# Kernel tuning notes

Measured on AMD Instinct MI355X. Metric: run time of the kernel, lower is better.

The kernel has to match this reference:

```python
import jax, jax.numpy as jnp
import numpy as np
import math

D_MODEL = 1024
D_STATE = 64
DT_MIN = 0.001
DT_MAX = 0.1
BATCH = 4
SEQLEN = 4096


def make_hippo_matrix(N):
    P = np.sqrt(1 + 2 * np.arange(N))
    A = P[:, np.newaxis] * P[np.newaxis, :]
    A = np.tril(A) - np.diag(np.arange(N))
    return jnp.asarray(-A, dtype=jnp.float32)


def setup_inputs() -> dict:
    key = jax.random.key(0)
    k_u, k_B, k_C, k_D, k_dt = jax.random.split(key, 5)
    u = jax.random.normal(k_u, (BATCH, SEQLEN, D_MODEL), dtype=jnp.float32)
    A = make_hippo_matrix(D_STATE)  # (N, N) HiPPO-LegS buffer
    B = jax.random.normal(k_B, (D_STATE, 1), dtype=jnp.float32)
    C = jax.random.normal(k_C, (1, D_STATE), dtype=jnp.float32)
    D = jax.random.normal(k_D, (1,), dtype=jnp.float32)
    log_dt = (jax.random.uniform(k_dt, (1,), dtype=jnp.float32)
              * (math.log(DT_MAX) - math.log(DT_MIN)) + math.log(DT_MIN))
    return {"u": u, "A": A, "B": B, "C": C, "D": D, "log_dt": log_dt}


def _forward(u, A, B, C, D, log_dt):
    n = A.shape[0]
    dt = jnp.exp(log_dt)[0]
    A_bar = jax.scipy.linalg.expm(dt * A)                     # (N, N)
    B_bar = jnp.linalg.solve(A, (A_bar - jnp.eye(n, dtype=A.dtype)) @ B)  # (N, 1)
    bvec = B_bar[:, 0]          # (N,)
    cvec = C[0]                 # (N,)
    d_scalar = D[0]
    # Faithful to source: only channel 0 of u drives the SSM.
    u0 = u[:, :, 0]             # (Bn, L)

    def step(x, u_t):
        # x: (Bn, N), u_t: (Bn,)
        x = x @ A_bar.T + u_t[:, None] * bvec
        y = x @ cvec + d_scalar * u_t   # (Bn,)
        return x, y

    x0 = jnp.zeros((u.shape[0], n), dtype=u.dtype)
    _, ys = jax.lax.scan(step, x0, jnp.swapaxes(u0, 0, 1))   # (L, Bn)
    # Scalar output broadcast across all H channels (matches torch expand)
    y = jnp.broadcast_to(jnp.swapaxes(ys, 0, 1)[:, :, None], u.shape)
    return y


def reference(u, A, B, C, D, log_dt):
    return _forward(u, A, B, C, D, log_dt)
```

## Files before the change

### kernel.cpp

```cpp
#include <hip/hip_runtime.h>


#define NT 256
#define MP 68
#define MB (64 * MP)

typedef __attribute__((ext_vector_type(8))) short v8s;
typedef __attribute__((ext_vector_type(4))) float v4f;

__device__ __forceinline__ unsigned short bf16r(float x) {
  union { float f; unsigned u; } v; v.f = x;
  unsigned r = v.u + 0x7fffu + ((v.u >> 16) & 1u);
  return (unsigned short)(r >> 16);
}
__device__ __forceinline__ float bf2f(unsigned short h) {
  union { unsigned u; float f; } v; v.u = ((unsigned)h) << 16;
  return v.f;
}
__device__ __forceinline__ void cvt4(const float4 f, ushort4* H, ushort4* L) {
  unsigned short h;
  h = bf16r(f.x); H->x = h; L->x = bf16r(f.x - bf2f(h));
  h = bf16r(f.y); H->y = h; L->y = bf16r(f.y - bf2f(h));
  h = bf16r(f.z); H->z = h; L->z = bf16r(f.z - bf2f(h));
  h = bf16r(f.w); H->w = h; L->w = bf16r(f.w - bf2f(h));
}

__device__ void mm(const float* Ag, const float* Bs, int bT,
                   float* Cd, int cpitch, float* Cd2,
                   int nrt, int nct, int rowbase, int colbase,
                   unsigned short* FRAG) {
  const int t = threadIdx.x;
  __syncthreads();
  for (int s0 = 0; s0 < 512; s0 += 256) {
    const int s = s0 + t;
    const int l = s & 63, Tq = s >> 6;
    const int mrow = (Tq >> 1) * 16 + (l & 15);
    const int kk = (Tq & 1) * 32 + (l >> 4) * 8;
    const float* ap = Ag + mrow * MP + kk;
    const float4 f0 = *(const float4*)ap;
    const float4 f1 = *(const float4*)(ap + 4);
    ushort4 H0, L0, H1, L1;
    cvt4(f0, &H0, &L0); cvt4(f1, &H1, &L1);
    *(ushort4*)(FRAG + s * 8)            = H0;
    *(ushort4*)(FRAG + s * 8 + 4)        = H1;
    *(ushort4*)(FRAG + 4096 + s * 8)     = L0;
    *(ushort4*)(FRAG + 4096 + s * 8 + 4) = L1;
    float4 g0, g1;
    if (bT) {
      const float* bp = Bs + mrow * MP + kk;
      g0 = *(const float4*)bp;
      g1 = *(const float4*)(bp + 4);
    } else {
      g0.x = Bs[(kk + 0) * MP + mrow]; g0.y = Bs[(kk + 1) * MP + mrow];
      g0.z = Bs[(kk + 2) * MP + mrow]; g0.w = Bs[(kk + 3) * MP + mrow];
      g1.x = Bs[(kk + 4) * MP + mrow]; g1.y = Bs[(kk + 5) * MP + mrow];
      g1.z = Bs[(kk + 6) * MP + mrow]; g1.w = Bs[(kk + 7) * MP + mrow];
    }
    cvt4(g0, &H0, &L0); cvt4(g1, &H1, &L1);
    *(ushort4*)(FRAG + 8192 + s * 8)      = H0;
    *(ushort4*)(FRAG + 8192 + s * 8 + 4)  = H1;
    *(ushort4*)(FRAG + 12288 + s * 8)     = L0;
    *(ushort4*)(FRAG + 12288 + s * 8 + 4) = L1;
  }
  __syncthreads();
  {
    const int w = t >> 6, l = t & 63;
    if (w < nrt) {
      const v8s Ah0 = *(const v8s*)(FRAG + ((w * 2 + 0) * 64 + l) * 8);
      const v8s Ah1 = *(const v8s*)(FRAG + ((w * 2 + 1) * 64 + l) * 8);
      const v8s Al0 = *(const v8s*)(FRAG + 4096 + ((w * 2 + 0) * 64 + l) * 8);
      const v8s Al1 = *(const v8s*)(FRAG + 4096 + ((w * 2 + 1) * 64 + l) * 8);
      for (int Cc = 0; Cc < nct; ++Cc) {
        const v8s Bh0 = *(const v8s*)(FRAG + 8192 + ((Cc * 2 + 0) * 64 + l) * 8);
        const v8s Bh1 = *(const v8s*)(FRAG + 8192 + ((Cc * 2 + 1) * 64 + l) * 8);
        const v8s Bl0 = *(const v8s*)(FRAG + 12288 + ((Cc * 2 + 0) * 64 + l) * 8);
        const v8s Bl1 = *(const v8s*)(FRAG + 12288 + ((Cc * 2 + 1) * 64 + l) * 8);
        const v4f z = {0.f, 0.f, 0.f, 0.f};
        v4f a0 = __builtin_amdgcn_mfma_f32_16x16x32_bf16(Ah0, Bh0, z, 0, 0, 0);
        a0 = __builtin_amdgcn_mfma_f32_16x16x32_bf16(Ah1, Bh1, a0, 0, 0, 0);
        v4f a1 = __builtin_amdgcn_mfma_f32_16x16x32_bf16(Ah0, Bl0, z, 0, 0, 0);
        a1 = __builtin_amdgcn_mfma_f32_16x16x32_bf16(Ah1, Bl1, a1, 0, 0, 0);
        v4f a2 = __builtin_amdgcn_mfma_f32_16x16x32_bf16(Al0, Bh0, z, 0, 0, 0);
        a2 = __builtin_amdgcn_mfma_f32_16x16x32_bf16(Al1, Bh1, a2, 0, 0, 0);
        const int col = colbase + Cc * 16 + (l & 15);
        const int r0 = rowbase + w * 16 + (l >> 4) * 4;
        const float o0 = a0[0] + a1[0] + a2[0];
        const float o1 = a0[1] + a1[1] + a2[1];
        const float o2 = a0[2] + a1[2] + a2[2];
        const float o3 = a0[3] + a1[3] + a2[3];
        Cd[(r0 + 0) * cpitch + col] = o0;
        Cd[(r0 + 1) * cpitch + col] = o1;
        Cd[(r0 + 2) * cpitch + col] = o2;
        Cd[(r0 + 3) * cpitch + col] = o3;
        if (Cd2) {
          Cd2[(r0 + 0) * MP + col] = o0;
          Cd2[(r0 + 1) * MP + col] = o1;
          Cd2[(r0 + 2) * MP + col] = o2;
          Cd2[(r0 + 3) * MP + col] = o3;
        }
      }
    }
  }
  __syncthreads();
}

__device__ __forceinline__ void mv64row(const float* M, const float* vin,
                                        float* vout, float* out2, int half) {
  const int t = threadIdx.x;
  __syncthreads();
  const int w = t >> 6, l = t & 63;
  const int row = w * 16 + (l >> 2), q = l & 3;
  const float* mp = M + row * MP + q * 16;
  const float* vp = vin + q * 16;
  float p = 0.f;
#pragma unroll
  for (int j = 0; j < 16; j += 4) {
    const float4 m = *(const float4*)(mp + j);
    p = fmaf(m.x, vp[j + 0], p);
    p = fmaf(m.y, vp[j + 1], p);
    p = fmaf(m.z, vp[j + 2], p);
    p = fmaf(m.w, vp[j + 3], p);
  }
  p += __shfl_xor(p, 1);
  p += __shfl_xor(p, 2);
  if (q == 0) {
    float s = half ? 0.5f * (p + vin[row]) : p;
    vout[row] = s;
    if (out2) out2[row] = s;
  }
  __syncthreads();
}

__device__ __forceinline__ void mv64colT(const float* M, const float* vin,
                                         float* vout, float* out2) {
  const int t = threadIdx.x;
  __syncthreads();
  const int w = t >> 6, l = t & 63;
  const int col = w * 16 + (l >> 2), q = l & 3;
  float p = 0.f;
#pragma unroll
  for (int j = 0; j < 16; ++j)
    p = fmaf(M[(q * 16 + j) * MP + col], vin[q * 16 + j], p);
  p += __shfl_xor(p, 1);
  p += __shfl_xor(p, 2);
  if (q == 0) {
    vout[col] = p;
    if (out2) out2[col] = p;
  }
  __syncthreads();
}

__device__ void buildG(float* dst, const float* X, const float* X2, const float* X3,
                       float c0, float c1, float c2, float c3, const float* addsrc) {
  const int t = threadIdx.x;
  __syncthreads();
  const int r = t >> 2, cb = (t & 3) * 16;
#pragma unroll
  for (int j = 0; j < 16; j += 4) {
    const int c = cb + j;
    const int e = r * MP + c;
    const float4 x1 = *(const float4*)(X + e);
    const float4 x2 = *(const float4*)(X2 + e);
    const float4 x3 = *(const float4*)(X3 + e);
    float4 v;
    v.x = fmaf(c1, x1.x, fmaf(c2, x2.x, c3 * x3.x));
    v.y = fmaf(c1, x1.y, fmaf(c2, x2.y, c3 * x3.y));
    v.z = fmaf(c1, x1.z, fmaf(c2, x2.z, c3 * x3.z));
    v.w = fmaf(c1, x1.w, fmaf(c2, x2.w, c3 * x3.w));
    if (r == c + 0) v.x += c0;
    if (r == c + 1) v.y += c0;
    if (r == c + 2) v.z += c0;
    if (r == c + 3) v.w += c0;
    if (addsrc) {
      const float4 a = *(const float4*)(addsrc + e);
      v.x += a.x; v.y += a.y; v.z += a.z; v.w += a.w;
    }
    *(float4*)(dst + e) = v;
  }
  __syncthreads();
}

__global__ __launch_bounds__(NT) void s4_setup(const float* __restrict__ u,
    const float* __restrict__ A, const float* __restrict__ Bv,
    const float* __restrict__ Cv, const float* __restrict__ logdt,
    float* __restrict__ ws) {
  if (blockIdx.x > 0) {
    const int idx = (blockIdx.x - 1) * NT + threadIdx.x;
    ws[4096 + idx] = u[(size_t)idx * 1024];
    return;
  }
  __shared__ __align__(16) float S0[MB];
  __shared__ __align__(16) unsigned short FRAG[16384];
  __shared__ float vB[64], v1[64], v2[64], v3[64], va[64], vb[64], vg[64];
  __shared__ int s_s;
  float* vscr = (float*)FRAG;

  const int t = threadIdx.x;
  float* kbuf = ws;
  float* gX   = ws + 20480;
  float* gX2  = ws + 24832;
  float* gX3  = ws + 29184;
  float* gU0  = ws + 33536;
  float* gU1  = ws + 37888;
  float* gBRT = ws + 42240;
  float* gCQT = ws + 46592;
  const float dt = expf(logdt[0]);

  const float invf[17] = {1.f, 1.f, 1.f / 2.f, 1.f / 6.f, 1.f / 24.f, 1.f / 120.f,
                          1.f / 720.f, 1.f / 5040.f, 1.f / 40320.f, 1.f / 362880.f,
                          1.f / 3628800.f, 1.f / 39916800.f, 1.f / 479001600.f,
                          1.f / 6.2270208e9f, 1.f / 8.71782912e10f,
                          1.f / 1.307674368e12f, 1.f / 2.0922789888e13f};

  {
    const int j = t & 63, w = t >> 6;
    float p = 0.f;
#pragma unroll
    for (int ii = 0; ii < 16; ++ii) p += fabsf(A[(w * 16 + ii) * 64 + j]);
    vscr[t] = p;
    __syncthreads();
    if (t < 64) {
      float cs = vscr[t] + vscr[64 + t] + vscr[128 + t] + vscr[192 + t];
      cs *= dt;
#pragma unroll
      for (int off = 32; off > 0; off >>= 1) cs = fmaxf(cs, __shfl_xor(cs, off));
      if (t == 0) {
        int s = 0;
        while (cs > 2.0f && s < 30) { cs *= 0.5f; ++s; }
        s_s = s;
      }
    }
    __syncthreads();
  }
  const int sq = s_s;
  const float scl = ldexpf(dt, -sq);

  {
    const int r = t >> 2, cb = (t & 3) * 16;
#pragma unroll
    for (int j = 0; j < 16; j += 4) {
      const float4 a4 = *(const float4*)(A + r * 64 + cb + j);
      float4 x;
      x.x = a4.x * scl; x.y = a4.y * scl; x.z = a4.z * scl; x.w = a4.w * scl;
      *(float4*)(S0 + r * MP + cb + j) = x;
      *(float4*)(gX + r * MP + cb + j) = x;
    }
    if (t < 64) vB[t] = Bv[t];
    __syncthreads();
  }

  mm(S0, S0, 0, S0, MP, gX2, 4, 4, 0, 0, FRAG);
  mm(gX, S0, 0, gX3, MP, nullptr, 4, 4, 0, 0, FRAG);
  mm(S0, S0, 0, S0, MP, nullptr, 4, 4, 0, 0, FRAG);

  mv64row(gX,  vB, v1, nullptr, 0);
  mv64row(gX2, vB, v2, nullptr, 0);
  mv64row(gX3, vB, v3, nullptr, 0);
  if (t < 64)
    va[t] = invf[13] * vB[t] + invf[14] * v1[t] + invf[15] * v2[t] + invf[16] * v3[t];
  __syncthreads();
  mv64row(S0, va, vb, nullptr, 0);
  if (t < 64)
    va[t] = invf[9] * vB[t] + invf[10] * v1[t] + invf[11] * v2[t] + invf[12] * v3[t] + vb[t];
  __syncthreads();
  mv64row(S0, va, vb, nullptr, 0);
  if (t < 64)
    va[t] = invf[5] * vB[t] + invf[6] * v1[t] + invf[7] * v2[t] + invf[8] * v3[t] + vb[t];
  __syncthreads();
  mv64row(S0, va, vb, nullptr, 0);
  if (t < 64)
    vg[t] = invf[1] * vB[t] + invf[2] * v1[t] + invf[3] * v2[t] + invf[4] * v3[t] + vb[t];
  __syncthreads();

  buildG(gU0, gX, gX2, gX3, invf[12], invf[13], invf[14], invf[15], nullptr);
  mm(gU0, S0, 0, gU1, MP, nullptr, 4, 4, 0, 0, FRAG);
  buildG(gU1, gX, gX2, gX3, invf[8], invf[9], invf[10], invf[11], gU1);
  mm(gU1, S0, 0, gU0, MP, nullptr, 4, 4, 0, 0, FRAG);
  buildG(gU0, gX, gX2, gX3, invf[4], invf[5], invf[6], invf[7], gU0);
  mm(gU0, S0, 0, S0, MP, nullptr, 4, 4, 0, 0, FRAG);
  buildG(S0, gX, gX2, gX3, invf[0], invf[1], invf[2], invf[3], S0);

  float* vcur = vg;
  float* vnxt = va;
  for (int it = 0; it < sq; ++it) {
    mv64row(S0, vcur, vnxt, nullptr, 1);
    { float* tmp = vcur; vcur = vnxt; vnxt = tmp; }
    mm(S0, S0, 0, S0, MP, nullptr, 4, 4, 0, 0, FRAG);
  }

  if (t < 64) {
    const float bb = dt * vcur[t];
    v1[t] = bb;
    gBRT[t] = bb;
  }
  __syncthreads();
  {
    float* vc = v1; float* vn = v2;
    for (int r = 1; r < 16; ++r) {
      mv64row(S0, vc, vn, gBRT + r * MP, 0);
      float* tmp = vc; vc = vn; vn = tmp;
    }
  }

  mm(S0, S0, 0, S0, MP, nullptr, 4, 4, 0, 0, FRAG);
  mm(S0, S0, 0, S0, MP, nullptr, 4, 4, 0, 0, FRAG);
  mm(S0, S0, 0, S0, MP, nullptr, 4, 4, 0, 0, FRAG);
  mm(S0, S0, 0, S0, MP, nullptr, 4, 4, 0, 0, FRAG);
  mm(gBRT, S0, 1, gBRT, MP, nullptr, 1, 4, 16, 0, FRAG);
  mm(S0, S0, 0, S0, MP, nullptr, 4, 4, 0, 0, FRAG);
  mm(gBRT, S0, 1, gBRT, MP, nullptr, 2, 4, 32, 0, FRAG);
  mm(S0, S0, 0, S0, MP, nullptr, 4, 4, 0, 0, FRAG);

  if (t < 64) {
    const float cc = Cv[t];
    v1[t] = cc;
    gCQT[t] = cc;
  }
  __syncthreads();
  {
    float* vc = v1; float* vn = v2;
    for (int qx = 1; qx < 16; ++qx) {
      mv64colT(S0, vc, vn, gCQT + qx * MP);
      float* tmp = vc; vc = vn; vn = tmp;
    }
  }

  mm(S0, S0, 0, S0, MP, nullptr, 4, 4, 0, 0, FRAG);
  mm(S0, S0, 0, S0, MP, nullptr, 4, 4, 0, 0, FRAG);
  mm(S0, S0, 0, S0, MP, nullptr, 4, 4, 0, 0, FRAG);
  mm(S0, S0, 0, S0, MP, nullptr, 4, 4, 0, 0, FRAG);
  mm(gCQT, S0, 0, gCQT, MP, nullptr, 1, 4, 16, 0, FRAG);
  mm(S0, S0, 0, S0, MP, nullptr, 4, 4, 0, 0, FRAG);
  mm(gCQT, S0, 0, gCQT, MP, nullptr, 2, 4, 32, 0, FRAG);

  mm(gCQT, gBRT, 1, kbuf, 64, nullptr, 4, 4, 0, 0, FRAG);
}

__global__ __launch_bounds__(256) void s4_out(const float* __restrict__ ws,
                                              const float* __restrict__ Dp,
                                              float* __restrict__ out) {
  const int bid = blockIdx.x;
  const int b = bid >> 10;
  const int t0 = (bid & 1023) << 2;
  const float* kb = ws;
  const float* ub = ws + 4096 + (b << 12);
  const int tid = threadIdx.x;

  float a0 = 0.f, a1 = 0.f, a2 = 0.f, a3 = 0.f;
  for (int s0 = tid << 2; s0 <= t0; s0 += 1024) {
    const float4 uv = *(const float4*)(ub + s0);
    const int b0 = t0 - s0;
    const float4 k0 = *(const float4*)(kb + b0);
    float4 k1 = make_float4(0.f, 0.f, 0.f, 0.f);
    if (b0 >= 4) k1 = *(const float4*)(kb + b0 - 4);
    a0 = fmaf(k0.x, uv.x, a0);
    a0 = fmaf(k1.w, uv.y, a0);
    a0 = fmaf(k1.z, uv.z, a0);
    a0 = fmaf(k1.y, uv.w, a0);
    a1 = fmaf(k0.y, uv.x, a1);
    a1 = fmaf(k0.x, uv.y, a1);
    a1 = fmaf(k1.w, uv.z, a1);
    a1 = fmaf(k1.z, uv.w, a1);
    a2 = fmaf(k0.z, uv.x, a2);
    a2 = fmaf(k0.y, uv.y, a2);
    a2 = fmaf(k0.x, uv.z, a2);
    a2 = fmaf(k1.w, uv.w, a2);
    a3 = fmaf(k0.w, uv.x, a3);
    a3 = fmaf(k0.z, uv.y, a3);
    a3 = fmaf(k0.y, uv.z, a3);
    a3 = fmaf(k0.x, uv.w, a3);
  }
#pragma unroll
  for (int off = 32; off > 0; off >>= 1) {
    a0 += __shfl_xor(a0, off);
    a1 += __shfl_xor(a1, off);
    a2 += __shfl_xor(a2, off);
    a3 += __shfl_xor(a3, off);
  }
  __shared__ float red[4][4];
  __shared__ float sy[4];
  if ((tid & 63) == 0) {
    const int w = tid >> 6;
    red[0][w] = a0; red[1][w] = a1; red[2][w] = a2; red[3][w] = a3;
  }
  __syncthreads();
  if (tid < 4)
    sy[tid] = red[tid][0] + red[tid][1] + red[tid][2] + red[tid][3] +
              Dp[0] * ub[t0 + tid];
  __syncthreads();
  const int row = tid >> 6, l = tid & 63;
  const float y = sy[row];
  const v4f y4 = {y, y, y, y};
  v4f* dst = (v4f*)(out + ((size_t)(b << 12) + t0 + row) * 1024);
  __builtin_nontemporal_store(y4, dst + l);
  __builtin_nontemporal_store(y4, dst + l + 64);
  __builtin_nontemporal_store(y4, dst + l + 128);
  __builtin_nontemporal_store(y4, dst + l + 192);
}

extern "C" void kernel_launch(void* const* d_in, const int* in_sizes, int n_in,
                              void* d_out, int out_size, void* d_ws, size_t ws_size,
                              hipStream_t stream) {
  const float* u  = (const float*)d_in[0];
  const float* A  = (const float*)d_in[1];
  const float* B  = (const float*)d_in[2];
  const float* C  = (const float*)d_in[3];
  const float* D  = (const float*)d_in[4];
  const float* ld = (const float*)d_in[5];
  float* ws = (float*)d_ws;

  s4_setup<<<65, NT, 0, stream>>>(u, A, B, C, ld, ws);
  s4_out<<<4096, 256, 0, stream>>>(ws, D, (float*)d_out);
}
```

Baseline: 187.4 us.

## Run setup expm chain in a single wavefront without block barriers

The serial setup block (matrix exponential via Taylor with squaring, plus building the B and C power tables) now runs on a single 64-lane wavefront. All intermediates stay in LDS rather than global workspace, so the many __syncthreads barriers and the FRAG staging copies disappear. MFMA operands are converted straight from LDS into registers. Each wave now does four times more MFMA and conversion work per matmul, trading parallelism for lower latency on a latency-bound critical path.

```diff
diff --git a/kernel.cpp b/kernel.cpp
--- a/kernel.cpp
+++ b/kernel.cpp
@@ -24,140 +24,117 @@
   h = bf16r(f.z); H->z = h; L->z = bf16r(f.z - bf2f(h));
   h = bf16r(f.w); H->w = h; L->w = bf16r(f.w - bf2f(h));
 }
-
-__device__ void mm(const float* Ag, const float* Bs, int bT,
-                   float* Cd, int cpitch, float* Cd2,
-                   int nrt, int nct, int rowbase, int colbase,
-                   unsigned short* FRAG) {
-  const int t = threadIdx.x;
-  __syncthreads();
-  for (int s0 = 0; s0 < 512; s0 += 256) {
-    const int s = s0 + t;
-    const int l = s & 63, Tq = s >> 6;
-    const int mrow = (Tq >> 1) * 16 + (l & 15);
-    const int kk = (Tq & 1) * 32 + (l >> 4) * 8;
-    const float* ap = Ag + mrow * MP + kk;
-    const float4 f0 = *(const float4*)ap;
-    const float4 f1 = *(const float4*)(ap + 4);
-    ushort4 H0, L0, H1, L1;
-    cvt4(f0, &H0, &L0); cvt4(f1, &H1, &L1);
-    *(ushort4*)(FRAG + s * 8)            = H0;
-    *(ushort4*)(FRAG + s * 8 + 4)        = H1;
-    *(ushort4*)(FRAG + 4096 + s * 8)     = L0;
-    *(ushort4*)(FRAG + 4096 + s * 8 + 4) = L1;
-    float4 g0, g1;
-    if (bT) {
-      const float* bp = Bs + mrow * MP + kk;
-      g0 = *(const float4*)bp;
-      g1 = *(const float4*)(bp + 4);
-    } else {
-      g0.x = Bs[(kk + 0) * MP + mrow]; g0.y = Bs[(kk + 1) * MP + mrow];
-      g0.z = Bs[(kk + 2) * MP + mrow]; g0.w = Bs[(kk + 3) * MP + mrow];
-      g1.x = Bs[(kk + 4) * MP + mrow]; g1.y = Bs[(kk + 5) * MP + mrow];
-      g1.z = Bs[(kk + 6) * MP + mrow]; g1.w = Bs[(kk + 7) * MP + mrow];
-    }
-    cvt4(g0, &H0, &L0); cvt4(g1, &H1, &L1);
-    *(ushort4*)(FRAG + 8192 + s * 8)      = H0;
-    *(ushort4*)(FRAG + 8192 + s * 8 + 4)  = H1;
-    *(ushort4*)(FRAG + 12288 + s * 8)     = L0;
-    *(ushort4*)(FRAG + 12288 + s * 8 + 4) = L1;
-  }
-  __syncthreads();
-  {
-    const int w = t >> 6, l = t & 63;
-    if (w < nrt) {
-      const v8s Ah0 = *(const v8s*)(FRAG + ((w * 2 + 0) * 64 + l) * 8);
-      const v8s Ah1 = *(const v8s*)(FRAG + ((w * 2 + 1) * 64 + l) * 8);
-      const v8s Al0 = *(const v8s*)(FRAG + 4096 + ((w * 2 + 0) * 64 + l) * 8);
-      const v8s Al1 = *(const v8s*)(FRAG + 4096 + ((w * 2 + 1) * 64 + l) * 8);
-      for (int Cc = 0; Cc < nct; ++Cc) {
-        const v8s Bh0 = *(const v8s*)(FRAG + 8192 + ((Cc * 2 + 0) * 64 + l) * 8);
-        const v8s Bh1 = *(const v8s*)(FRAG + 8192 + ((Cc * 2 + 1) * 64 + l) * 8);
-        const v8s Bl0 = *(const v8s*)(FRAG + 12288 + ((Cc * 2 + 0) * 64 + l) * 8);
-        const v8s Bl1 = *(const v8s*)(FRAG + 12288 + ((Cc * 2 + 1) * 64 + l) * 8);
-        const v4f z = {0.f, 0.f, 0.f, 0.f};
-        v4f a0 = __builtin_amdgcn_mfma_f32_16x16x32_bf16(Ah0, Bh0, z, 0, 0, 0);
-        a0 = __builtin_amdgcn_mfma_f32_16x16x32_bf16(Ah1, Bh1, a0, 0, 0, 0);
-        v4f a1 = __builtin_amdgcn_mfma_f32_16x16x32_bf16(Ah0, Bl0, z, 0, 0, 0);
-        a1 = __builtin_amdgcn_mfma_f32_16x16x32_bf16(Ah1, Bl1, a1, 0, 0, 0);
-        v4f a2 = __builtin_amdgcn_mfma_f32_16x16x32_bf16(Al0, Bh0, z, 0, 0, 0);
-        a2 = __builtin_amdgcn_mfma_f32_16x16x32_bf16(Al1, Bh1, a2, 0, 0, 0);
-        const int col = colbase + Cc * 16 + (l & 15);
-        const int r0 = rowbase + w * 16 + (l >> 4) * 4;
-        const float o0 = a0[0] + a1[0] + a2[0];
-        const float o1 = a0[1] + a1[1] + a2[1];
-        const float o2 = a0[2] + a1[2] + a2[2];
-        const float o3 = a0[3] + a1[3] + a2[3];
-        Cd[(r0 + 0) * cpitch + col] = o0;
-        Cd[(r0 + 1) * cpitch + col] = o1;
-        Cd[(r0 + 2) * cpitch + col] = o2;
-        Cd[(r0 + 3) * cpitch + col] = o3;
-        if (Cd2) {
-          Cd2[(r0 + 0) * MP + col] = o0;
-          Cd2[(r0 + 1) * MP + col] = o1;
-          Cd2[(r0 + 2) * MP + col] = o2;
-          Cd2[(r0 + 3) * MP + col] = o3;
-        }
+__device__ __forceinline__ void cvt8(const float4 f0, const float4 f1,
+                                     v8s* H, v8s* L) {
+  union { v8s v; ushort4 u[2]; } Hu, Lu;
+  cvt4(f0, &Hu.u[0], &Lu.u[0]);
+  cvt4(f1, &Hu.u[1], &Lu.u[1]);
+  *H = Hu.v; *L = Lu.v;
+}
+
+template<int NRT, int BT>
+__device__ __attribute__((noinline)) void mm1w(const int l, const float* As,
+    const float* Bs, float* Cd, const int cpitch, const int rowbase,
+    float* Cd2) {
+  const int m = l & 15;
+  const int g = l >> 4;
+  v8s Ah[NRT][2], Al[NRT][2];
+#pragma unroll
+  for (int rt = 0; rt < NRT; ++rt)
+#pragma unroll
+    for (int h = 0; h < 2; ++h) {
+      const float* ap = As + (rt * 16 + m) * MP + h * 32 + g * 8;
+      cvt8(*(const float4*)ap, *(const float4*)(ap + 4), &Ah[rt][h], &Al[rt][h]);
+    }
+  v4f acc[NRT][4];
+#pragma unroll
+  for (int rt = 0; rt < NRT; ++rt)
+#pragma unroll
+    for (int ct = 0; ct < 4; ++ct) acc[rt][ct] = (v4f){0.f, 0.f, 0.f, 0.f};
+#pragma unroll
+  for (int ct = 0; ct < 4; ++ct) {
+    v8s Bh[2], Bl[2];
+#pragma unroll
+    for (int h = 0; h < 2; ++h) {
+      float4 g0, g1;
+      if (BT) {
+        const float* bp = Bs + (ct * 16 + m) * MP + h * 32 + g * 8;
+        g0 = *(const float4*)bp;
+        g1 = *(const float4*)(bp + 4);
+      } else {
+        const int kb = h * 32 + g * 8;
+        const int cc = ct * 16 + m;
+        g0.x = Bs[(kb + 0) * MP + cc]; g0.y = Bs[(kb + 1) * MP + cc];
+        g0.z = Bs[(kb + 2) * MP + cc]; g0.w = Bs[(kb + 3) * MP + cc];
+        g1.x = Bs[(kb + 4) * MP + cc]; g1.y = Bs[(kb + 5) * MP + cc];
+        g1.z = Bs[(kb + 6) * MP + cc]; g1.w = Bs[(kb + 7) * MP + cc];
       }
-    }
-  }
-  __syncthreads();
-}
-
-__device__ __forceinline__ void mv64row(const float* M, const float* vin,
-                                        float* vout, float* out2, int half) {
-  const int t = threadIdx.x;
-  __syncthreads();
-  const int w = t >> 6, l = t & 63;
-  const int row = w * 16 + (l >> 2), q = l & 3;
-  const float* mp = M + row * MP + q * 16;
-  const float* vp = vin + q * 16;
-  float p = 0.f;
-#pragma unroll
-  for (int j = 0; j < 16; j += 4) {
-    const float4 m = *(const float4*)(mp + j);
-    p = fmaf(m.x, vp[j + 0], p);
-    p = fmaf(m.y, vp[j + 1], p);
-    p = fmaf(m.z, vp[j + 2], p);
-    p = fmaf(m.w, vp[j + 3], p);
-  }
-  p += __shfl_xor(p, 1);
-  p += __shfl_xor(p, 2);
-  if (q == 0) {
-    float s = half ? 0.5f * (p + vin[row]) : p;
-    vout[row] = s;
-    if (out2) out2[row] = s;
-  }
-  __syncthreads();
-}
-
-__device__ __forceinline__ void mv64colT(const float* M, const float* vin,
-                                         float* vout, float* out2) {
-  const int t = threadIdx.x;
-  __syncthreads();
-  const int w = t >> 6, l = t & 63;
-  const int col = w * 16 + (l >> 2), q = l & 3;
-  float p = 0.f;
-#pragma unroll
-  for (int j = 0; j < 16; ++j)
-    p = fmaf(M[(q * 16 + j) * MP + col], vin[q * 16 + j], p);
-  p += __shfl_xor(p, 1);
-  p += __shfl_xor(p, 2);
-  if (q == 0) {
-    vout[col] = p;
-    if (out2) out2[col] = p;
-  }
-  __syncthreads();
-}
-
-__device__ void buildG(float* dst, const float* X, const float* X2, const float* X3,
-                       float c0, float c1, float c2, float c3, const float* addsrc) {
-  const int t = threadIdx.x;
-  __syncthreads();
-  const int r = t >> 2, cb = (t & 3) * 16;
-#pragma unroll
-  for (int j = 0; j < 16; j += 4) {
-    const int c = cb + j;
+      cvt8(g0, g1, &Bh[h], &Bl[h]);
+    }
+#pragma unroll
+    for (int rt = 0; rt < NRT; ++rt) {
+      v4f a = acc[rt][ct];
+      a = __builtin_amdgcn_mfma_f32_16x16x32_bf16(Ah[rt][0], Bh[0], a, 0, 0, 0);
+      a = __builtin_amdgcn_mfma_f32_16x16x32_bf16(Ah[rt][1], Bh[1], a, 0, 0, 0);
+      a = __builtin_amdgcn_mfma_f32_16x16x32_bf16(Ah[rt][0], Bl[0], a, 0, 0, 0);
+      a = __builtin_amdgcn_mfma_f32_16x16x32_bf16(Ah[rt][1], Bl[1], a, 0, 0, 0);
+      a = __builtin_amdgcn_mfma_f32_16x16x32_bf16(Al[rt][0], Bh[0], a, 0, 0, 0);
+      a = __builtin_amdgcn_mfma_f32_16x16x32_bf16(Al[rt][1], Bh[1], a, 0, 0, 0);
+      acc[rt][ct] = a;
+    }
+  }
+#pragma unroll
+  for (int rt = 0; rt < NRT; ++rt)
+#pragma unroll
+    for (int ct = 0; ct < 4; ++ct) {
+      const int col = ct * 16 + m;
+      const int r0 = rowbase + rt * 16 + g * 4;
+#pragma unroll
+      for (int i = 0; i < 4; ++i) {
+        const float o = acc[rt][ct][i];
+        Cd[(size_t)(r0 + i) * cpitch + col] = o;
+        if (Cd2) Cd2[(r0 + i) * MP + col] = o;
+      }
+    }
+}
+
+__device__ __forceinline__ float dotrow1w(const int l, const float* M,
+                                          const float* VV) {
+  const float* mp = M + l * MP;
+  float pa = 0.f, pb = 0.f, pc = 0.f, pd = 0.f;
+#pragma unroll
+  for (int jq = 0; jq < 16; ++jq) {
+    const float4 m4 = *(const float4*)(mp + jq * 4);
+    const float4 w4 = *(const float4*)(VV + jq * 4);
+    pa = fmaf(m4.x, w4.x, pa);
+    pb = fmaf(m4.y, w4.y, pb);
+    pc = fmaf(m4.z, w4.z, pc);
+    pd = fmaf(m4.w, w4.w, pd);
+  }
+  return (pa + pb) + (pc + pd);
+}
+
+__device__ __forceinline__ float dotcol1w(const int l, const float* M,
+                                          const float* VV) {
+  float pa = 0.f, pb = 0.f, pc = 0.f, pd = 0.f;
+#pragma unroll
+  for (int j = 0; j < 64; j += 4) {
+    pa = fmaf(M[(j + 0) * MP + l], VV[j + 0], pa);
+    pb = fmaf(M[(j + 1) * MP + l], VV[j + 1], pb);
+    pc = fmaf(M[(j + 2) * MP + l], VV[j + 2], pc);
+    pd = fmaf(M[(j + 3) * MP + l], VV[j + 3], pd);
+  }
+  return (pa + pb) + (pc + pd);
+}
+
+__device__ __forceinline__ void buildG1w(const int l, float* dst, const float* X,
+    const float* X2, const float* X3, const float c0, const float c1,
+    const float c2, const float c3, const float* addsrc) {
+#pragma unroll
+  for (int i = 0; i < 16; ++i) {
+    const int f = l + (i << 6);
+    const int r = f >> 4;
+    const int c = (f & 15) * 4;
     const int e = r * MP + c;
     const float4 x1 = *(const float4*)(X + e);
     const float4 x2 = *(const float4*)(X2 + e);
@@ -177,10 +154,9 @@
     }
     *(float4*)(dst + e) = v;
   }
-  __syncthreads();
-}
-
-__global__ __launch_bounds__(NT) void s4_setup(const float* __restrict__ u,
+}
+
+__global__ __launch_bounds__(NT, 1) void s4_setup(const float* __restrict__ u,
     const float* __restrict__ A, const float* __restrict__ Bv,
     const float* __restrict__ Cv, const float* __restrict__ logdt,
     float* __restrict__ ws) {
@@ -189,21 +165,21 @@
     ws[4096 + idx] = u[(size_t)idx * 1024];
     return;
   }
-  __shared__ __align__(16) float S0[MB];
-  __shared__ __align__(16) unsigned short FRAG[16384];
-  __shared__ float vB[64], v1[64], v2[64], v3[64], va[64], vb[64], vg[64];
-  __shared__ int s_s;
-  float* vscr = (float*)FRAG;
+  __shared__ __align__(16) float SH[MB];
+  __shared__ __align__(16) float SXs[MB];
+  __shared__ __align__(16) float SX2s[MB];
+  __shared__ __align__(16) float SX3s[MB];
+  __shared__ __align__(16) float SU0s[MB];
+  __shared__ __align__(16) float SU1s[MB];
+  __shared__ __align__(16) float VV[64];
 
   const int t = threadIdx.x;
+  if (t >= 64) return;
+  const int l = t;
+
   float* kbuf = ws;
-  float* gX   = ws + 20480;
-  float* gX2  = ws + 24832;
-  float* gX3  = ws + 29184;
-  float* gU0  = ws + 33536;
-  float* gU1  = ws + 37888;
-  float* gBRT = ws + 42240;
-  float* gCQT = ws + 46592;
+  float* SBRT = SU0s;
+  float* SCQT = SU1s;
   const float dt = expf(logdt[0]);
 
   const float invf[17] = {1.f, 1.f, 1.f / 2.f, 1.f / 6.f, 1.f / 24.f, 1.f / 120.f,
@@ -212,128 +188,103 @@
                           1.f / 6.2270208e9f, 1.f / 8.71782912e10f,
                           1.f / 1.307674368e12f, 1.f / 2.0922789888e13f};
 
-  {
-    const int j = t & 63, w = t >> 6;
-    float p = 0.f;
-#pragma unroll
-    for (int ii = 0; ii < 16; ++ii) p += fabsf(A[(w * 16 + ii) * 64 + j]);
-    vscr[t] = p;
-    __syncthreads();
-    if (t < 64) {
-      float cs = vscr[t] + vscr[64 + t] + vscr[128 + t] + vscr[192 + t];
-      cs *= dt;
-#pragma unroll
-      for (int off = 32; off > 0; off >>= 1) cs = fmaxf(cs, __shfl_xor(cs, off));
-      if (t == 0) {
-        int s = 0;
-        while (cs > 2.0f && s < 30) { cs *= 0.5f; ++s; }
-        s_s = s;
-      }
-    }
-    __syncthreads();
-  }
-  const int sq = s_s;
+#pragma unroll
+  for (int i = 0; i < 16; ++i) {
+    const int f = l + (i << 6);
+    const float4 a4 = *(const float4*)(A + f * 4);
+    *(float4*)(SH + (f >> 4) * MP + (f & 15) * 4) = a4;
+  }
+
+  float csum = 0.f;
+#pragma unroll 8
+  for (int r = 0; r < 64; ++r) csum += fabsf(SH[r * MP + l]);
+  float cs = csum * dt;
+#pragma unroll
+  for (int off = 32; off > 0; off >>= 1) cs = fmaxf(cs, __shfl_xor(cs, off));
+  int sq = 0;
+  while (cs > 2.0f && sq < 30) { cs *= 0.5f; ++sq; }
   const float scl = ldexpf(dt, -sq);
 
-  {
-    const int r = t >> 2, cb = (t & 3) * 16;
-#pragma unroll
-    for (int j = 0; j < 16; j += 4) {
-      const float4 a4 = *(const float4*)(A + r * 64 + cb + j);
-      float4 x;
-      x.x = a4.x * scl; x.y = a4.y * scl; x.z = a4.z * scl; x.w = a4.w * scl;
-      *(float4*)(S0 + r * MP + cb + j) = x;
-      *(float4*)(gX + r * MP + cb + j) = x;
-    }
-    if (t < 64) vB[t] = Bv[t];
-    __syncthreads();
-  }
-
-  mm(S0, S0, 0, S0, MP, gX2, 4, 4, 0, 0, FRAG);
-  mm(gX, S0, 0, gX3, MP, nullptr, 4, 4, 0, 0, FRAG);
-  mm(S0, S0, 0, S0, MP, nullptr, 4, 4, 0, 0, FRAG);
-
-  mv64row(gX,  vB, v1, nullptr, 0);
-  mv64row(gX2, vB, v2, nullptr, 0);
-  mv64row(gX3, vB, v3, nullptr, 0);
-  if (t < 64)
-    va[t] = invf[13] * vB[t] + invf[14] * v1[t] + invf[15] * v2[t] + invf[16] * v3[t];
-  __syncthreads();
-  mv64row(S0, va, vb, nullptr, 0);
-  if (t < 64)
-    va[t] = invf[9] * vB[t] + invf[10] * v1[t] + invf[11] * v2[t] + invf[12] * v3[t] + vb[t];
-  __syncthreads();
-  mv64row(S0, va, vb, nullptr, 0);
-  if (t < 64)
-    va[t] = invf[5] * vB[t] + invf[6] * v1[t] + invf[7] * v2[t] + invf[8] * v3[t] + vb[t];
-  __syncthreads();
-  mv64row(S0, va, vb, nullptr, 0);
-  if (t < 64)
-    vg[t] = invf[1] * vB[t] + invf[2] * v1[t] + invf[3] * v2[t] + invf[4] * v3[t] + vb[t];
-  __syncthreads();
-
-  buildG(gU0, gX, gX2, gX3, invf[12], invf[13], invf[14], invf[15], nullptr);
-  mm(gU0, S0, 0, gU1, MP, nullptr, 4, 4, 0, 0, FRAG);
-  buildG(gU1, gX, gX2, gX3, invf[8], invf[9], invf[10], invf[11], gU1);
-  mm(gU1, S0, 0, gU0, MP, nullptr, 4, 4, 0, 0, FRAG);
-  buildG(gU0, gX, gX2, gX3, invf[4], invf[5], invf[6], invf[7], gU0);
-  mm(gU0, S0, 0, S0, MP, nullptr, 4, 4, 0, 0, FRAG);
-  buildG(S0, gX, gX2, gX3, invf[0], invf[1], invf[2], invf[3], S0);
-
-  float* vcur = vg;
-  float* vnxt = va;
+#pragma unroll
+  for (int i = 0; i < 16; ++i) {
+    const int f = l + (i << 6);
+    const int e = (f >> 4) * MP + (f & 15) * 4;
+    float4 x = *(const float4*)(SH + e);
+    x.x *= scl; x.y *= scl; x.z *= scl; x.w *= scl;
+    *(float4*)(SH + e) = x;
+    *(float4*)(SXs + e) = x;
+  }
+  const float vBr = Bv[l];
+
+  mm1w<4, 0>(l, SH, SH, SH, MP, 0, SX2s);
+  mm1w<4, 0>(l, SXs, SH, SX3s, MP, 0, nullptr);
+  mm1w<4, 0>(l, SH, SH, SH, MP, 0, nullptr);
+
+  VV[l] = vBr;
+  const float v1r = dotrow1w(l, SXs, VV);
+  const float v2r = dotrow1w(l, SX2s, VV);
+  const float v3r = dotrow1w(l, SX3s, VV);
+  float var = invf[13] * vBr + invf[14] * v1r + invf[15] * v2r + invf[16] * v3r;
+  VV[l] = var;
+  float vbr = dotrow1w(l, SH, VV);
+  var = invf[9] * vBr + invf[10] * v1r + invf[11] * v2r + invf[12] * v3r + vbr;
+  VV[l] = var;
+  vbr = dotrow1w(l, SH, VV);
+  var = invf[5] * vBr + invf[6] * v1r + invf[7] * v2r + invf[8] * v3r + vbr;
+  VV[l] = var;
+  vbr = dotrow1w(l, SH, VV);
+  float vgr = invf[1] * vBr + invf[2] * v1r + invf[3] * v2r + invf[4] * v3r + vbr;
+
+  buildG1w(l, SU0s, SXs, SX2s, SX3s, invf[12], invf[13], invf[14], invf[15], nullptr);
+  mm1w<4, 0>(l, SU0s, SH, SU1s, MP, 0, nullptr);
+  buildG1w(l, SU1s, SXs, SX2s, SX3s, invf[8], invf[9], invf[10], invf[11], SU1s);
+  mm1w<4, 0>(l, SU1s, SH, SU0s, MP, 0, nullptr);
+  buildG1w(l, SU0s, SXs, SX2s, SX3s, invf[4], invf[5], invf[6], invf[7], SU0s);
+  mm1w<4, 0>(l, SU0s, SH, SH, MP, 0, nullptr);
+  buildG1w(l, SH, SXs, SX2s, SX3s, invf[0], invf[1], invf[2], invf[3], SH);
+
+  float cur = vgr;
   for (int it = 0; it < sq; ++it) {
-    mv64row(S0, vcur, vnxt, nullptr, 1);
-    { float* tmp = vcur; vcur = vnxt; vnxt = tmp; }
-    mm(S0, S0, 0, S0, MP, nullptr, 4, 4, 0, 0, FRAG);
-  }
-
-  if (t < 64) {
-    const float bb = dt * vcur[t];
-    v1[t] = bb;
-    gBRT[t] = bb;
-  }
-  __syncthreads();
-  {
-    float* vc = v1; float* vn = v2;
-    for (int r = 1; r < 16; ++r) {
-      mv64row(S0, vc, vn, gBRT + r * MP, 0);
-      float* tmp = vc; vc = vn; vn = tmp;
-    }
-  }
-
-  mm(S0, S0, 0, S0, MP, nullptr, 4, 4, 0, 0, FRAG);
-  mm(S0, S0, 0, S0, MP, nullptr, 4, 4, 0, 0, FRAG);
-  mm(S0, S0, 0, S0, MP, nullptr, 4, 4, 0, 0, FRAG);
-  mm(S0, S0, 0, S0, MP, nullptr, 4, 4, 0, 0, FRAG);
-  mm(gBRT, S0, 1, gBRT, MP, nullptr, 1, 4, 16, 0, FRAG);
-  mm(S0, S0, 0, S0, MP, nullptr, 4, 4, 0, 0, FRAG);
-  mm(gBRT, S0, 1, gBRT, MP, nullptr, 2, 4, 32, 0, FRAG);
-  mm(S0, S0, 0, S0, MP, nullptr, 4, 4, 0, 0, FRAG);
-
-  if (t < 64) {
-    const float cc = Cv[t];
-    v1[t] = cc;
-    gCQT[t] = cc;
-  }
-  __syncthreads();
-  {
-    float* vc = v1; float* vn = v2;
-    for (int qx = 1; qx < 16; ++qx) {
-      mv64colT(S0, vc, vn, gCQT + qx * MP);
-      float* tmp = vc; vc = vn; vn = tmp;
-    }
-  }
-
-  mm(S0, S0, 0, S0, MP, nullptr, 4, 4, 0, 0, FRAG);
-  mm(S0, S0, 0, S0, MP, nullptr, 4, 4, 0, 0, FRAG);
-  mm(S0, S0, 0, S0, MP, nullptr, 4, 4, 0, 0, FRAG);
-  mm(S0, S0, 0, S0, MP, nullptr, 4, 4, 0, 0, FRAG);
-  mm(gCQT, S0, 0, gCQT, MP, nullptr, 1, 4, 16, 0, FRAG);
-  mm(S0, S0, 0, S0, MP, nullptr, 4, 4, 0, 0, FRAG);
-  mm(gCQT, S0, 0, gCQT, MP, nullptr, 2, 4, 32, 0, FRAG);
-
-  mm(gCQT, gBRT, 1, kbuf, 64, nullptr, 4, 4, 0, 0, FRAG);
+    VV[l] = cur;
+    const float p = dotrow1w(l, SH, VV);
+    cur = 0.5f * (p + cur);
+    mm1w<4, 0>(l, SH, SH, SH, MP, 0, nullptr);
+  }
+
+  float bcur = dt * cur;
+  SBRT[l] = bcur;
+  for (int r = 1; r < 16; ++r) {
+    VV[l] = bcur;
+    bcur = dotrow1w(l, SH, VV);
+    SBRT[r * MP + l] = bcur;
+  }
+
+  mm1w<4, 0>(l, SH, SH, SH, MP, 0, nullptr);
+  mm1w<4, 0>(l, SH, SH, SH, MP, 0, nullptr);
+  mm1w<4, 0>(l, SH, SH, SH, MP, 0, nullptr);
+  mm1w<4, 0>(l, SH, SH, SH, MP, 0, nullptr);
+  mm1w<1, 1>(l, SBRT, SH, SBRT, MP, 16, nullptr);
+  mm1w<4, 0>(l, SH, SH, SH, MP, 0, nullptr);
+  mm1w<2, 1>(l, SBRT, SH, SBRT, MP, 32, nullptr);
+  mm1w<4, 0>(l, SH, SH, SH, MP, 0, nullptr);
+
+  float ccur = Cv[l];
+  SCQT[l] = ccur;
+  for (int qx = 1; qx < 16; ++qx) {
+    VV[l] = ccur;
+    ccur = dotcol1w(l, SH, VV);
+    SCQT[qx * MP + l] = ccur;
+  }
+
+  mm1w<4, 0>(l, SH, SH, SH, MP, 0, nullptr);
+  mm1w<4, 0>(l, SH, SH, SH, MP, 0, nullptr);
+  mm1w<4, 0>(l, SH, SH, SH, MP, 0, nullptr);
+  mm1w<4, 0>(l, SH, SH, SH, MP, 0, nullptr);
+  mm1w<1, 0>(l, SCQT, SH, SCQT, MP, 16, nullptr);
+  mm1w<4, 0>(l, SH, SH, SH, MP, 0, nullptr);
+  mm1w<2, 0>(l, SCQT, SH, SCQT, MP, 32, nullptr);
+
+  mm1w<4, 1>(l, SCQT, SBRT, kbuf, 64, 0, nullptr);
 }
 
 __global__ __launch_bounds__(256) void s4_out(const float* __restrict__ ws,
@@ -388,14 +339,14 @@
     sy[tid] = red[tid][0] + red[tid][1] + red[tid][2] + red[tid][3] +
               Dp[0] * ub[t0 + tid];
   __syncthreads();
-  const int row = tid >> 6, l = tid & 63;
+  const int row = tid >> 6, lx = tid & 63;
   const float y = sy[row];
   const v4f y4 = {y, y, y, y};
   v4f* dst = (v4f*)(out + ((size_t)(b << 12) + t0 + row) * 1024);
-  __builtin_nontemporal_store(y4, dst + l);
-  __builtin_nontemporal_store(y4, dst + l + 64);
-  __builtin_nontemporal_store(y4, dst + l + 128);
-  __builtin_nontemporal_store(y4, dst + l + 192);
+  __builtin_nontemporal_store(y4, dst + lx);
+  __builtin_nontemporal_store(y4, dst + lx + 64);
+  __builtin_nontemporal_store(y4, dst + lx + 128);
+  __builtin_nontemporal_store(y4, dst + lx + 192);
 }
 
 extern "C" void kernel_launch(void* const* d_in, const int* in_sizes, int n_in,
```

Result: slower. 255.2 us (+36.2%).
